# Performance work log

Hardware: AMD Instinct MI355X
Metric: run time of the kernel (lower is better)

Reference implementation:

```python
import jax, jax.numpy as jnp
import numpy as np

N_ATOM = 4096
NHEADS = 8
C_PER_HEAD = 64
BLOCK_SIZE = 128
LOCAL_WINDOW = 512


def setup_inputs() -> dict:
    key = jax.random.key(0)
    k1, k2, k3, k4 = jax.random.split(key, 4)
    q = jax.random.normal(k1, (N_ATOM, NHEADS, C_PER_HEAD), dtype=jnp.float32)
    k = jax.random.normal(k2, (N_ATOM, NHEADS, C_PER_HEAD), dtype=jnp.float32)
    v = jax.random.normal(k3, (N_ATOM, NHEADS, C_PER_HEAD), dtype=jnp.float32)
    pair_bias = jax.random.normal(k4, (N_ATOM, N_ATOM, NHEADS), dtype=jnp.float32)
    return {"q": q, "k": k, "v": v, "pair_bias": pair_bias}


def reference(q, k, v, pair_bias):
    # Local block-sparse attention: banded blockmask with blocks_per_side
    # = max(1, local_window // block_size) blocks on each side of the diagonal.
    # NOTE: pair_bias is accepted by the original forward but never used
    # (it is not passed to block_sparse_attn_func), so it is ignored here.
    N, H, D = q.shape
    B = BLOCK_SIZE
    bps = max(1, LOCAL_WINDOW // BLOCK_SIZE)  # blocks per side = 4
    nrow = N // B  # N is a multiple of block_size here
    scale = jnp.asarray(D, q.dtype) ** -0.5  # softmax_scale=None -> 1/sqrt(d)

    qb = q.reshape(nrow, B, H, D)
    kb = k.reshape(nrow, B, H, D)
    vb = v.reshape(nrow, B, H, D)

    offs = jnp.arange(-bps, bps + 1)                      # [W], W = 2*bps+1
    cols = jnp.arange(nrow)[:, None] + offs[None, :]      # [nrow, W]
    valid = (cols >= 0) & (cols < nrow)                   # band edge mask
    colsc = jnp.clip(cols, 0, nrow - 1)

    kg = kb[colsc]  # [nrow, W, B, H, D] -- only band blocks gathered
    vg = vb[colsc]

    # scores: [nrow, H, B, W, B]
    scores = jnp.einsum('rihd,rwjhd->rhiwj', qb, kg) * scale
    neg_inf = jnp.asarray(-jnp.inf, scores.dtype)
    scores = jnp.where(valid[:, None, None, :, None], scores, neg_inf)

    p = jax.nn.softmax(scores.reshape(nrow, H, B, -1), axis=-1)
    p = p.reshape(scores.shape)

    out = jnp.einsum('rhiwj,rwjhd->rihd', p, vg)  # [nrow, B, H, D]
    return out.reshape(N, H, D)
```

## Files before the change

kernel.cpp:

```cpp
#include <hip/hip_runtime.h>
#include <hip/hip_bf16.h>

#define NATOM 4096
#define NH 8
#define DIMD 64
#define BLK 128
#define NROW 32
#define BPS 4
#define ROWSTRIDE (NH * DIMD)
#define SCALE 0.125f
#define L2E 1.4426950408889634f

#define K_LD 72
#define V_LD 136
#define P_LD 136

#define HEAD_ELEMS (NATOM * DIMD)
#define WS_NEEDED  (2u * NH * HEAD_ELEMS * 2u)

typedef __attribute__((ext_vector_type(8))) short bf16x8;
typedef __attribute__((ext_vector_type(4))) float f32x4;
typedef __attribute__((ext_vector_type(4))) unsigned int u32x4;

__device__ __forceinline__ short f2bf(float x) {
    unsigned int u = __builtin_bit_cast(unsigned int, x);
    unsigned int r = (u + 0x7fffu + ((u >> 16) & 1u)) >> 16;
    return (short)r;
}
__device__ __forceinline__ unsigned int cvtpk(float lo, float hi) {
    unsigned int r;
    asm("v_cvt_pk_bf16_f32 %0, %1, %2" : "=v"(r) : "v"(lo), "v"(hi));
    return r;
}

extern "C" __global__ __launch_bounds__(256)
void prep_kernel(const float* __restrict__ k, const float* __restrict__ v,
                 short* __restrict__ Kb, short* __restrict__ Vt)
{
    __shared__ short Tr[DIMD * V_LD];
    const int bid  = blockIdx.x;
    const int h    = bid & 7;
    const int part = bid >> 3;
    const int t    = threadIdx.x;

    if (part < 32) {
        const int nb = part;
        #pragma unroll
        for (int i = 0; i < 4; ++i) {
            int idx = i * 256 + t;
            int row = idx >> 3;
            int d0  = (idx & 7) * 8;
            const float* src = k + (size_t)(nb * BLK + row) * ROWSTRIDE + h * DIMD + d0;
            float4 a = *(const float4*)src;
            float4 c = *(const float4*)(src + 4);
            bf16x8 f;
            f[0] = f2bf(a.x); f[1] = f2bf(a.y); f[2] = f2bf(a.z); f[3] = f2bf(a.w);
            f[4] = f2bf(c.x); f[5] = f2bf(c.y); f[6] = f2bf(c.z); f[7] = f2bf(c.w);
            *(bf16x8*)(Kb + (size_t)h * HEAD_ELEMS + (size_t)(nb * BLK + row) * DIMD + d0) = f;
        }
    } else {
        const int nb = part - 32;
        const int vd = t & 63;
        const int g  = t >> 6;
        const float* vp = v + (size_t)(nb * BLK) * ROWSTRIDE + h * DIMD + vd;
        #pragma unroll
        for (int i = 0; i < 8; ++i) {
            int n4 = i * 16 + g * 4;
            const float* vr = vp + (size_t)n4 * ROWSTRIDE;
            short4 s4;
            s4.x = f2bf(vr[0 * ROWSTRIDE]);
            s4.y = f2bf(vr[1 * ROWSTRIDE]);
            s4.z = f2bf(vr[2 * ROWSTRIDE]);
            s4.w = f2bf(vr[3 * ROWSTRIDE]);
            *(short4*)&Tr[vd * V_LD + n4] = s4;
        }
        __syncthreads();
        #pragma unroll
        for (int i = 0; i < 4; ++i) {
            int s  = i * 256 + t;
            int d  = s >> 4;
            int c8 = (s & 15) * 8;
            int kc = c8 >> 5;
            int l2 = (c8 >> 3) & 3;
            int kA = kc * 32 + l2 * 4;
            short4 a  = *(const short4*)&Tr[d * V_LD + kA];
            short4 c4 = *(const short4*)&Tr[d * V_LD + kA + 16];
            bf16x8 f;
            f[0] = a.x;  f[1] = a.y;  f[2] = a.z;  f[3] = a.w;
            f[4] = c4.x; f[5] = c4.y; f[6] = c4.z; f[7] = c4.w;
            *(bf16x8*)(Vt + (size_t)h * HEAD_ELEMS + (size_t)d * NATOM + nb * BLK + c8) = f;
        }
    }
}

extern "C" __global__ __launch_bounds__(256)
void bsattn_main(const float* __restrict__ q,
                 const short* __restrict__ Kb,
                 const short* __restrict__ Vt,
                 float* __restrict__ out)
{
    __shared__ short Ksh[2][BLK * K_LD];
    __shared__ short Vsh[2][DIMD * V_LD];

    const int bid = blockIdx.x;
    const int h   = bid & 7;
    const int br  = bid >> 3;
    const int r   = br >> 1;
    const int t   = threadIdx.x;
    const int w   = t >> 6;
    const int lane = t & 63;
    const int lr = lane >> 4;
    const int lc = lane & 15;

    const int qbase = br * 64 + w * 16;
    const float* qp = q + (size_t)(qbase + lc) * ROWSTRIDE + h * DIMD + lr * 8;
    bf16x8 qf[2];
    #pragma unroll
    for (int kc = 0; kc < 2; ++kc) {
        float4 a = *(const float4*)(qp + kc * 32);
        float4 b = *(const float4*)(qp + kc * 32 + 4);
        bf16x8 f;
        f[0] = f2bf(a.x * (SCALE * L2E)); f[1] = f2bf(a.y * (SCALE * L2E));
        f[2] = f2bf(a.z * (SCALE * L2E)); f[3] = f2bf(a.w * (SCALE * L2E));
        f[4] = f2bf(b.x * (SCALE * L2E)); f[5] = f2bf(b.y * (SCALE * L2E));
        f[6] = f2bf(b.z * (SCALE * L2E)); f[7] = f2bf(b.w * (SCALE * L2E));
        qf[kc] = f;
    }
    bf16x8 onesA;
    #pragma unroll
    for (int i = 0; i < 8; ++i) onesA[i] = (short)0x3F80;

    const short* kbase = Kb + (size_t)h * HEAD_ELEMS;
    const short* vbase = Vt + (size_t)h * HEAD_ELEMS;

    f32x4 acc[4] = {};
    f32x4 lacc = {};

    const int kb0 = (r - BPS > 0) ? (r - BPS) : 0;
    const int kb1 = (r + BPS < NROW - 1) ? (r + BPS) : (NROW - 1);

    const short* kg = kbase + (size_t)kb0 * BLK * DIMD;
    const short* vg = vbase + (size_t)kb0 * BLK;
    bf16x8 kpre[4], vpre[4];

#define LOADREGS()                                                              \
    {                                                                           \
        _Pragma("unroll")                                                       \
        for (int i = 0; i < 4; ++i) {                                           \
            int s = i * 256 + t;                                                \
            kpre[i] = *(const bf16x8*)(kg + (size_t)(s >> 3) * DIMD + (s & 7) * 8); \
            vpre[i] = *(const bf16x8*)(vg + (size_t)(s >> 4) * NATOM + (s & 15) * 8); \
        }                                                                       \
        kg += BLK * DIMD; vg += BLK;                                            \
    }

#define STAGE(buf)                                                              \
    {                                                                           \
        _Pragma("unroll")                                                       \
        for (int i = 0; i < 4; ++i) {                                           \
            int s = i * 256 + t;                                                \
            *(bf16x8*)&Ksh[buf][(s >> 3) * K_LD + (s & 7) * 8] = kpre[i];       \
            *(bf16x8*)&Vsh[buf][(s >> 4) * V_LD + (s & 15) * 8] = vpre[i];      \
        }                                                                       \
    }

    LOADREGS();
    STAGE(0);
    if (kb0 < kb1) LOADREGS();
    __syncthreads();

    int cur = 0;
    for (int kb = kb0; kb <= kb1; ++kb) {
        const short* ks = &Ksh[cur][0];
        const short* vs = &Vsh[cur][0];

        f32x4 s[8];
        __builtin_amdgcn_s_setprio(1);
        #pragma unroll
        for (int mt = 0; mt < 8; ++mt) {
            f32x4 z = {};
            #pragma unroll
            for (int kc = 0; kc < 2; ++kc) {
                bf16x8 kf = *(const bf16x8*)&ks[(mt * 16 + lc) * K_LD + kc * 32 + lr * 8];
                z = __builtin_amdgcn_mfma_f32_16x16x32_bf16(kf, qf[kc], z, 0, 0, 0);
            }
            s[mt] = z;
        }
        __builtin_amdgcn_s_setprio(0);

        #pragma unroll
        for (int mt = 0; mt < 8; ++mt) {
            #pragma unroll
            for (int e = 0; e < 4; ++e)
                s[mt][e] = __builtin_amdgcn_exp2f(s[mt][e]);
        }

        bf16x8 pf[4];
        #pragma unroll
        for (int kc = 0; kc < 4; ++kc) {
            u32x4 pk;
            pk[0] = cvtpk(s[2 * kc][0],     s[2 * kc][1]);
            pk[1] = cvtpk(s[2 * kc][2],     s[2 * kc][3]);
            pk[2] = cvtpk(s[2 * kc + 1][0], s[2 * kc + 1][1]);
            pk[3] = cvtpk(s[2 * kc + 1][2], s[2 * kc + 1][3]);
            pf[kc] = __builtin_bit_cast(bf16x8, pk);
        }

        if (kb < kb1) {
            STAGE(cur ^ 1);
            if (kb + 1 < kb1) LOADREGS();
        }

        __builtin_amdgcn_s_setprio(1);
        #pragma unroll
        for (int dn = 0; dn < 4; ++dn) {
            f32x4 o = acc[dn];
            #pragma unroll
            for (int kc = 0; kc < 4; ++kc) {
                bf16x8 vf = *(const bf16x8*)&vs[(dn * 16 + lc) * V_LD + kc * 32 + lr * 8];
                o = __builtin_amdgcn_mfma_f32_16x16x32_bf16(vf, pf[kc], o, 0, 0, 0);
            }
            acc[dn] = o;
        }
        #pragma unroll
        for (int kc = 0; kc < 4; ++kc)
            lacc = __builtin_amdgcn_mfma_f32_16x16x32_bf16(onesA, pf[kc], lacc, 0, 0, 0);
        __builtin_amdgcn_s_setprio(0);

        __syncthreads();
        cur ^= 1;
    }

    float inv = 1.0f / lacc[0];
    float* orow = out + (size_t)(qbase + lc) * ROWSTRIDE + h * DIMD;
    #pragma unroll
    for (int dn = 0; dn < 4; ++dn) {
        f32x4 rv;
        rv[0] = acc[dn][0] * inv; rv[1] = acc[dn][1] * inv;
        rv[2] = acc[dn][2] * inv; rv[3] = acc[dn][3] * inv;
        *(float4*)(orow + dn * 16 + lr * 4) = *(float4*)&rv;
    }
#undef LOADREGS
#undef STAGE
}

extern "C" __global__ __launch_bounds__(512)
void bsattn_fallback(const float* __restrict__ q,
                     const float* __restrict__ k,
                     const float* __restrict__ v,
                     float* __restrict__ out)
{
    __shared__ short Ksh[BLK * K_LD];
    __shared__ short Vsh[DIMD * V_LD];
    __shared__ short Psh[8][16 * P_LD];

    const int r = blockIdx.x;
    const int h = blockIdx.y;
    const int t = threadIdx.x;
    const int w = t >> 6;
    const int lane = t & 63;
    const int lr = lane >> 4;
    const int lc = lane & 15;

    const int krow = t >> 4;
    const int kcol = (t & 15) * 4;
    const int vd  = t & 63;
    const int vkg = t >> 6;

    const int qrow_l = w * 16 + lc;
    const float* qp = q + (size_t)(r * BLK + qrow_l) * ROWSTRIDE + h * DIMD + lr * 8;
    bf16x8 qf[2];
    #pragma unroll
    for (int kc = 0; kc < 2; ++kc) {
        float4 a = *(const float4*)(qp + kc * 32);
        float4 b = *(const float4*)(qp + kc * 32 + 4);
        bf16x8 f;
        f[0] = f2bf(a.x); f[1] = f2bf(a.y); f[2] = f2bf(a.z); f[3] = f2bf(a.w);
        f[4] = f2bf(b.x); f[5] = f2bf(b.y); f[6] = f2bf(b.z); f[7] = f2bf(b.w);
        qf[kc] = f;
    }

    f32x4 acc[4] = {};
    float m_run[4], l_run[4];
    #pragma unroll
    for (int i = 0; i < 4; ++i) { m_run[i] = -1e30f; l_run[i] = 0.0f; }

    const int kb0 = (r - BPS > 0) ? (r - BPS) : 0;
    const int kb1 = (r + BPS < NROW - 1) ? (r + BPS) : (NROW - 1);

    for (int kb = kb0; kb <= kb1; ++kb) {
        __syncthreads();
        const float* kp = k + (size_t)(kb * BLK) * ROWSTRIDE + h * DIMD;
        const float* vp = v + (size_t)(kb * BLK) * ROWSTRIDE + h * DIMD;

        #pragma unroll
        for (int i = 0; i < 4; ++i) {
            float4 kv = *(const float4*)(kp + (size_t)(i * 32 + krow) * ROWSTRIDE + kcol);
            short4 ks;
            ks.x = f2bf(kv.x); ks.y = f2bf(kv.y); ks.z = f2bf(kv.z); ks.w = f2bf(kv.w);
            *(short4*)&Ksh[(i * 32 + krow) * K_LD + kcol] = ks;

            const float* vr = vp + (size_t)(i * 32 + vkg * 4) * ROWSTRIDE + vd;
            short4 vs;
            vs.x = f2bf(vr[0 * ROWSTRIDE]);
            vs.y = f2bf(vr[1 * ROWSTRIDE]);
            vs.z = f2bf(vr[2 * ROWSTRIDE]);
            vs.w = f2bf(vr[3 * ROWSTRIDE]);
            *(short4*)&Vsh[vd * V_LD + i * 32 + vkg * 4] = vs;
        }
        __syncthreads();

        f32x4 s[8];
        #pragma unroll
        for (int n = 0; n < 8; ++n) {
            f32x4 z = {};
            #pragma unroll
            for (int kc = 0; kc < 2; ++kc) {
                bf16x8 kf = *(const bf16x8*)&Ksh[(n * 16 + lc) * K_LD + kc * 32 + lr * 8];
                z = __builtin_amdgcn_mfma_f32_16x16x32_bf16(qf[kc], kf, z, 0, 0, 0);
            }
            s[n] = z * SCALE;
        }

        #pragma unroll
        for (int rr = 0; rr < 4; ++rr) {
            float mx = s[0][rr];
            #pragma unroll
            for (int n = 1; n < 8; ++n) mx = fmaxf(mx, s[n][rr]);
            #pragma unroll
            for (int off = 1; off < 16; off <<= 1)
                mx = fmaxf(mx, __shfl_xor(mx, off, 64));
            float mnew = fmaxf(m_run[rr], mx);
            float al = exp2f((m_run[rr] - mnew) * L2E);
            m_run[rr] = mnew;
            float sum = 0.0f;
            #pragma unroll
            for (int n = 0; n < 8; ++n) {
                float p = exp2f((s[n][rr] - mnew) * L2E);
                s[n][rr] = p;
                sum += p;
            }
            #pragma unroll
            for (int off = 1; off < 16; off <<= 1)
                sum += __shfl_xor(sum, off, 64);
            l_run[rr] = l_run[rr] * al + sum;
            #pragma unroll
            for (int dn = 0; dn < 4; ++dn) acc[dn][rr] *= al;
        }

        short* pw = &Psh[w][0];
        #pragma unroll
        for (int n = 0; n < 8; ++n) {
            #pragma unroll
            for (int rr = 0; rr < 4; ++rr) {
                pw[(lr * 4 + rr) * P_LD + n * 16 + lc] = f2bf(s[n][rr]);
            }
        }

        #pragma unroll
        for (int dn = 0; dn < 4; ++dn) {
            f32x4 o = acc[dn];
            #pragma unroll
            for (int kc = 0; kc < 4; ++kc) {
                bf16x8 pf = *(const bf16x8*)&pw[lc * P_LD + kc * 32 + lr * 8];
                bf16x8 vf = *(const bf16x8*)&Vsh[(dn * 16 + lc) * V_LD + kc * 32 + lr * 8];
                o = __builtin_amdgcn_mfma_f32_16x16x32_bf16(pf, vf, o, 0, 0, 0);
            }
            acc[dn] = o;
        }
    }

    float* op = out + (size_t)(r * BLK + w * 16) * ROWSTRIDE + h * DIMD;
    #pragma unroll
    for (int rr = 0; rr < 4; ++rr) {
        float inv = 1.0f / l_run[rr];
        float* orow = op + (size_t)(lr * 4 + rr) * ROWSTRIDE;
        #pragma unroll
        for (int dn = 0; dn < 4; ++dn) {
            orow[dn * 16 + lc] = acc[dn][rr] * inv;
        }
    }
}

extern "C" void kernel_launch(void* const* d_in, const int* in_sizes, int n_in,
                              void* d_out, int out_size, void* d_ws, size_t ws_size,
                              hipStream_t stream) {
    const float* q = (const float*)d_in[0];
    const float* k = (const float*)d_in[1];
    const float* v = (const float*)d_in[2];
    float* out = (float*)d_out;

    if (ws_size >= (size_t)WS_NEEDED) {
        short* Kb = (short*)d_ws;
        short* Vt = Kb + (size_t)NH * HEAD_ELEMS;
        prep_kernel<<<512, 256, 0, stream>>>(k, v, Kb, Vt);
        bsattn_main<<<512, 256, 0, stream>>>(q, Kb, Vt, out);
    } else {
        bsattn_fallback<<<dim3(NROW, NH), 512, 0, stream>>>(q, k, v, out);
    }
}
```

Measured before the change: 28.26 us.

## Switch main attention kernel to 32x32x16 MFMA with full 128-row query blocks

Replaces the 16x16x32 MFMA tiling with 32x32x16 tiles, so each workgroup handles a whole 128-row query block (4 waves x 32 rows) and the grid is halved to 256 workgroups. K/V in shared memory switch from padded layouts to XOR-swizzled layouts, and the prep kernel's V transpose order is changed to match the new fragment layout. The row sum is now accumulated from exp values in registers instead of a ones-matrix MFMA. Fewer workgroups halves redundant K/V tile loads, but the 256-workgroup grid may underfill the GPU's CUs.

New measurement: 30.16 us. 6.7% more time.

```diff
diff --git a/kernel.cpp b/kernel.cpp
--- a/kernel.cpp
+++ b/kernel.cpp
@@ -11,15 +11,16 @@
 #define SCALE 0.125f
 #define L2E 1.4426950408889634f
 
-#define K_LD 72
 #define V_LD 136
 #define P_LD 136
+#define K_LDF 72
 
 #define HEAD_ELEMS (NATOM * DIMD)
 #define WS_NEEDED  (2u * NH * HEAD_ELEMS * 2u)
 
 typedef __attribute__((ext_vector_type(8))) short bf16x8;
 typedef __attribute__((ext_vector_type(4))) float f32x4;
+typedef __attribute__((ext_vector_type(16))) float f32x16;
 typedef __attribute__((ext_vector_type(4))) unsigned int u32x4;
 
 __device__ __forceinline__ short f2bf(float x) {
@@ -79,12 +80,11 @@
         for (int i = 0; i < 4; ++i) {
             int s  = i * 256 + t;
             int d  = s >> 4;
-            int c8 = (s & 15) * 8;
-            int kc = c8 >> 5;
-            int l2 = (c8 >> 3) & 3;
-            int kA = kc * 32 + l2 * 4;
+            int cc = s & 15;
+            int c8 = cc * 8;
+            int kA = (cc >> 1) * 16 + (cc & 1) * 4;
             short4 a  = *(const short4*)&Tr[d * V_LD + kA];
-            short4 c4 = *(const short4*)&Tr[d * V_LD + kA + 16];
+            short4 c4 = *(const short4*)&Tr[d * V_LD + kA + 8];
             bf16x8 f;
             f[0] = a.x;  f[1] = a.y;  f[2] = a.z;  f[3] = a.w;
             f[4] = c4.x; f[5] = c4.y; f[6] = c4.z; f[7] = c4.w;
@@ -93,32 +93,32 @@
     }
 }
 
-extern "C" __global__ __launch_bounds__(256)
+extern "C" __global__ __launch_bounds__(256, 1)
 void bsattn_main(const float* __restrict__ q,
                  const short* __restrict__ Kb,
                  const short* __restrict__ Vt,
                  float* __restrict__ out)
 {
-    __shared__ short Ksh[2][BLK * K_LD];
-    __shared__ short Vsh[2][DIMD * V_LD];
+    __shared__ short Ksh[2][BLK * DIMD];
+    __shared__ short Vsh[2][DIMD * BLK];
 
     const int bid = blockIdx.x;
     const int h   = bid & 7;
-    const int br  = bid >> 3;
-    const int r   = br >> 1;
+    const int rb  = bid >> 3;
     const int t   = threadIdx.x;
     const int w   = t >> 6;
     const int lane = t & 63;
-    const int lr = lane >> 4;
-    const int lc = lane & 15;
-
-    const int qbase = br * 64 + w * 16;
-    const float* qp = q + (size_t)(qbase + lc) * ROWSTRIDE + h * DIMD + lr * 8;
-    bf16x8 qf[2];
+    const int lc  = lane & 31;
+    const int hi  = lane >> 5;
+
+    const int qrow = rb * BLK + w * 32 + lc;
+    const float* qp = q + (size_t)qrow * ROWSTRIDE + h * DIMD;
+    bf16x8 qf[4];
     #pragma unroll
-    for (int kc = 0; kc < 2; ++kc) {
-        float4 a = *(const float4*)(qp + kc * 32);
-        float4 b = *(const float4*)(qp + kc * 32 + 4);
+    for (int kc = 0; kc < 4; ++kc) {
+        const float* p = qp + kc * 16 + hi * 8;
+        float4 a = *(const float4*)p;
+        float4 b = *(const float4*)(p + 4);
         bf16x8 f;
         f[0] = f2bf(a.x * (SCALE * L2E)); f[1] = f2bf(a.y * (SCALE * L2E));
         f[2] = f2bf(a.z * (SCALE * L2E)); f[3] = f2bf(a.w * (SCALE * L2E));
@@ -126,42 +126,41 @@
         f[6] = f2bf(b.z * (SCALE * L2E)); f[7] = f2bf(b.w * (SCALE * L2E));
         qf[kc] = f;
     }
-    bf16x8 onesA;
-    #pragma unroll
-    for (int i = 0; i < 8; ++i) onesA[i] = (short)0x3F80;
 
     const short* kbase = Kb + (size_t)h * HEAD_ELEMS;
     const short* vbase = Vt + (size_t)h * HEAD_ELEMS;
 
-    f32x4 acc[4] = {};
-    f32x4 lacc = {};
-
-    const int kb0 = (r - BPS > 0) ? (r - BPS) : 0;
-    const int kb1 = (r + BPS < NROW - 1) ? (r + BPS) : (NROW - 1);
-
-    const short* kg = kbase + (size_t)kb0 * BLK * DIMD;
-    const short* vg = vbase + (size_t)kb0 * BLK;
+    f32x16 oacc[2] = {};
+    float sv = 0.0f;
+
+    const int kb0 = (rb - BPS > 0) ? (rb - BPS) : 0;
+    const int kb1 = (rb + BPS < NROW - 1) ? (rb + BPS) : (NROW - 1);
+
+    const short* kgp = kbase + (size_t)kb0 * BLK * DIMD;
+    const short* vgp = vbase + (size_t)kb0 * BLK;
     bf16x8 kpre[4], vpre[4];
 
-#define LOADREGS()                                                              \
-    {                                                                           \
-        _Pragma("unroll")                                                       \
-        for (int i = 0; i < 4; ++i) {                                           \
-            int s = i * 256 + t;                                                \
-            kpre[i] = *(const bf16x8*)(kg + (size_t)(s >> 3) * DIMD + (s & 7) * 8); \
-            vpre[i] = *(const bf16x8*)(vg + (size_t)(s >> 4) * NATOM + (s & 15) * 8); \
-        }                                                                       \
-        kg += BLK * DIMD; vg += BLK;                                            \
-    }
-
-#define STAGE(buf)                                                              \
-    {                                                                           \
-        _Pragma("unroll")                                                       \
-        for (int i = 0; i < 4; ++i) {                                           \
-            int s = i * 256 + t;                                                \
-            *(bf16x8*)&Ksh[buf][(s >> 3) * K_LD + (s & 7) * 8] = kpre[i];       \
-            *(bf16x8*)&Vsh[buf][(s >> 4) * V_LD + (s & 15) * 8] = vpre[i];      \
-        }                                                                       \
+#define LOADREGS()                                                               \
+    {                                                                            \
+        _Pragma("unroll")                                                        \
+        for (int i = 0; i < 4; ++i) {                                            \
+            int idx = i * 256 + t;                                               \
+            kpre[i] = *(const bf16x8*)(kgp + (size_t)(idx >> 3) * DIMD + (idx & 7) * 8);   \
+            vpre[i] = *(const bf16x8*)(vgp + (size_t)(idx >> 4) * NATOM + (idx & 15) * 8); \
+        }                                                                        \
+        kgp += BLK * DIMD; vgp += BLK;                                           \
+    }
+
+#define STAGE(buf)                                                               \
+    {                                                                            \
+        _Pragma("unroll")                                                        \
+        for (int i = 0; i < 4; ++i) {                                            \
+            int idx = i * 256 + t;                                               \
+            int kr = idx >> 3, kch = idx & 7;                                    \
+            *(bf16x8*)&Ksh[buf][kr * DIMD + ((kch ^ (kr & 7)) << 3)] = kpre[i];  \
+            int vd = idx >> 4, vch = idx & 15;                                   \
+            *(bf16x8*)&Vsh[buf][vd * BLK + ((vch ^ (vd & 7)) << 3)] = vpre[i];   \
+        }                                                                        \
     }
 
     LOADREGS();
@@ -174,36 +173,40 @@
         const short* ks = &Ksh[cur][0];
         const short* vs = &Vsh[cur][0];
 
-        f32x4 s[8];
+        f32x16 sA[4];
         __builtin_amdgcn_s_setprio(1);
         #pragma unroll
-        for (int mt = 0; mt < 8; ++mt) {
-            f32x4 z = {};
-            #pragma unroll
-            for (int kc = 0; kc < 2; ++kc) {
-                bf16x8 kf = *(const bf16x8*)&ks[(mt * 16 + lc) * K_LD + kc * 32 + lr * 8];
-                z = __builtin_amdgcn_mfma_f32_16x16x32_bf16(kf, qf[kc], z, 0, 0, 0);
-            }
-            s[mt] = z;
+        for (int mt = 0; mt < 4; ++mt) {
+            f32x16 z = {};
+            #pragma unroll
+            for (int kc = 0; kc < 4; ++kc) {
+                int row = mt * 32 + lc;
+                bf16x8 kf = *(const bf16x8*)&ks[row * DIMD + (((2 * kc + hi) ^ (row & 7)) << 3)];
+                z = __builtin_amdgcn_mfma_f32_32x32x16_bf16(kf, qf[kc], z, 0, 0, 0);
+            }
+            sA[mt] = z;
         }
         __builtin_amdgcn_s_setprio(0);
 
         #pragma unroll
-        for (int mt = 0; mt < 8; ++mt) {
-            #pragma unroll
-            for (int e = 0; e < 4; ++e)
-                s[mt][e] = __builtin_amdgcn_exp2f(s[mt][e]);
-        }
-
-        bf16x8 pf[4];
-        #pragma unroll
-        for (int kc = 0; kc < 4; ++kc) {
+        for (int mt = 0; mt < 4; ++mt) {
+            #pragma unroll
+            for (int e = 0; e < 16; ++e) {
+                float p = __builtin_amdgcn_exp2f(sA[mt][e]);
+                sA[mt][e] = p;
+                sv += p;
+            }
+        }
+
+        bf16x8 pf[8];
+        #pragma unroll
+        for (int kb16 = 0; kb16 < 8; ++kb16) {
+            int mt = kb16 >> 1, base = (kb16 & 1) * 8;
             u32x4 pk;
-            pk[0] = cvtpk(s[2 * kc][0],     s[2 * kc][1]);
-            pk[1] = cvtpk(s[2 * kc][2],     s[2 * kc][3]);
-            pk[2] = cvtpk(s[2 * kc + 1][0], s[2 * kc + 1][1]);
-            pk[3] = cvtpk(s[2 * kc + 1][2], s[2 * kc + 1][3]);
-            pf[kc] = __builtin_bit_cast(bf16x8, pk);
+            #pragma unroll
+            for (int w2 = 0; w2 < 4; ++w2)
+                pk[w2] = cvtpk(sA[mt][base + 2 * w2], sA[mt][base + 2 * w2 + 1]);
+            pf[kb16] = __builtin_bit_cast(bf16x8, pk);
         }
 
         if (kb < kb1) {
@@ -213,32 +216,36 @@
 
         __builtin_amdgcn_s_setprio(1);
         #pragma unroll
-        for (int dn = 0; dn < 4; ++dn) {
-            f32x4 o = acc[dn];
-            #pragma unroll
-            for (int kc = 0; kc < 4; ++kc) {
-                bf16x8 vf = *(const bf16x8*)&vs[(dn * 16 + lc) * V_LD + kc * 32 + lr * 8];
-                o = __builtin_amdgcn_mfma_f32_16x16x32_bf16(vf, pf[kc], o, 0, 0, 0);
-            }
-            acc[dn] = o;
-        }
-        #pragma unroll
-        for (int kc = 0; kc < 4; ++kc)
-            lacc = __builtin_amdgcn_mfma_f32_16x16x32_bf16(onesA, pf[kc], lacc, 0, 0, 0);
+        for (int dmt = 0; dmt < 2; ++dmt) {
+            f32x16 o = oacc[dmt];
+            #pragma unroll
+            for (int kb16 = 0; kb16 < 8; ++kb16) {
+                int row = dmt * 32 + lc;
+                bf16x8 vf = *(const bf16x8*)&vs[row * BLK + (((2 * kb16 + hi) ^ (row & 7)) << 3)];
+                o = __builtin_amdgcn_mfma_f32_32x32x16_bf16(vf, pf[kb16], o, 0, 0, 0);
+            }
+            oacc[dmt] = o;
+        }
         __builtin_amdgcn_s_setprio(0);
 
         __syncthreads();
         cur ^= 1;
     }
 
-    float inv = 1.0f / lacc[0];
-    float* orow = out + (size_t)(qbase + lc) * ROWSTRIDE + h * DIMD;
+    float l = sv + __shfl_xor(sv, 32, 64);
+    float inv = 1.0f / l;
+    float* orow = out + (size_t)qrow * ROWSTRIDE + h * DIMD;
     #pragma unroll
-    for (int dn = 0; dn < 4; ++dn) {
-        f32x4 rv;
-        rv[0] = acc[dn][0] * inv; rv[1] = acc[dn][1] * inv;
-        rv[2] = acc[dn][2] * inv; rv[3] = acc[dn][3] * inv;
-        *(float4*)(orow + dn * 16 + lr * 4) = *(float4*)&rv;
+    for (int dmt = 0; dmt < 2; ++dmt) {
+        #pragma unroll
+        for (int g = 0; g < 4; ++g) {
+            float4 rv;
+            rv.x = oacc[dmt][4 * g + 0] * inv;
+            rv.y = oacc[dmt][4 * g + 1] * inv;
+            rv.z = oacc[dmt][4 * g + 2] * inv;
+            rv.w = oacc[dmt][4 * g + 3] * inv;
+            *(float4*)(orow + dmt * 32 + g * 8 + hi * 4) = rv;
+        }
     }
 #undef LOADREGS
 #undef STAGE
@@ -250,7 +257,7 @@
                      const float* __restrict__ v,
                      float* __restrict__ out)
 {
-    __shared__ short Ksh[BLK * K_LD];
+    __shared__ short Ksh[BLK * K_LDF];
     __shared__ short Vsh[DIMD * V_LD];
     __shared__ short Psh[8][16 * P_LD];
 
@@ -298,7 +305,7 @@
             float4 kv = *(const float4*)(kp + (size_t)(i * 32 + krow) * ROWSTRIDE + kcol);
             short4 ks;
             ks.x = f2bf(kv.x); ks.y = f2bf(kv.y); ks.z = f2bf(kv.z); ks.w = f2bf(kv.w);
-            *(short4*)&Ksh[(i * 32 + krow) * K_LD + kcol] = ks;
+            *(short4*)&Ksh[(i * 32 + krow) * K_LDF + kcol] = ks;
 
             const float* vr = vp + (size_t)(i * 32 + vkg * 4) * ROWSTRIDE + vd;
             short4 vs;
@@ -316,7 +323,7 @@
             f32x4 z = {};
             #pragma unroll
             for (int kc = 0; kc < 2; ++kc) {
-                bf16x8 kf = *(const bf16x8*)&Ksh[(n * 16 + lc) * K_LD + kc * 32 + lr * 8];
+                bf16x8 kf = *(const bf16x8*)&Ksh[(n * 16 + lc) * K_LDF + kc * 32 + lr * 8];
                 z = __builtin_amdgcn_mfma_f32_16x16x32_bf16(qf[kc], kf, z, 0, 0, 0);
             }
             s[n] = z * SCALE;
@@ -362,9 +369,9 @@
             f32x4 o = acc[dn];
             #pragma unroll
             for (int kc = 0; kc < 4; ++kc) {
-                bf16x8 pf = *(const bf16x8*)&pw[lc * P_LD + kc * 32 + lr * 8];
+                bf16x8 pfr = *(const bf16x8*)&pw[lc * P_LD + kc * 32 + lr * 8];
                 bf16x8 vf = *(const bf16x8*)&Vsh[(dn * 16 + lc) * V_LD + kc * 32 + lr * 8];
-                o = __builtin_amdgcn_mfma_f32_16x16x32_bf16(pf, vf, o, 0, 0, 0);
+                o = __builtin_amdgcn_mfma_f32_16x16x32_bf16(pfr, vf, o, 0, 0, 0);
             }
             acc[dn] = o;
         }
@@ -394,7 +401,7 @@
         short* Kb = (short*)d_ws;
         short* Vt = Kb + (size_t)NH * HEAD_ELEMS;
         prep_kernel<<<512, 256, 0, stream>>>(k, v, Kb, Vt);
-        bsattn_main<<<512, 256, 0, stream>>>(q, Kb, Vt, out);
+        bsattn_main<<<256, 256, 0, stream>>>(q, Kb, Vt, out);
     } else {
         bsattn_fallback<<<dim3(NROW, NH), 512, 0, stream>>>(q, k, v, out);
     }
```

## Stream K/V tiles into LDS with global_load_lds using XOR-swizzled prepacked layout

Applied to the files above, without the earlier changes.

The prep kernel now writes K and transposed V in a per-tile layout with an XOR swizzle of 16-byte chunks. The main kernel can then copy whole tiles straight into LDS with global_load_lds, with no register staging and no padding. Loads for tile kb+2 are issued after the barrier into the buffer just consumed. LDS reads apply the matching XOR swizzle to avoid bank conflicts. This removes the VGPR round-trip and the LDS store instructions, but adds a full vmcnt(0) drain each iteration.

After: 27.09 us. 1.04x faster.

```diff
diff --git a/kernel.cpp b/kernel.cpp
--- a/kernel.cpp
+++ b/kernel.cpp
@@ -11,9 +11,10 @@
 #define SCALE 0.125f
 #define L2E 1.4426950408889634f
 
-#define K_LD 72
+#define TILE_EL (BLK * DIMD)
 #define V_LD 136
 #define P_LD 136
+#define K_LDF 72
 
 #define HEAD_ELEMS (NATOM * DIMD)
 #define WS_NEEDED  (2u * NH * HEAD_ELEMS * 2u)
@@ -31,6 +32,9 @@
     unsigned int r;
     asm("v_cvt_pk_bf16_f32 %0, %1, %2" : "=v"(r) : "v"(lo), "v"(hi));
     return r;
+}
+__device__ __forceinline__ void drain_gll() {
+    asm volatile("s_waitcnt vmcnt(0)" ::: "memory");
 }
 
 extern "C" __global__ __launch_bounds__(256)
@@ -49,14 +53,17 @@
         for (int i = 0; i < 4; ++i) {
             int idx = i * 256 + t;
             int row = idx >> 3;
-            int d0  = (idx & 7) * 8;
-            const float* src = k + (size_t)(nb * BLK + row) * ROWSTRIDE + h * DIMD + d0;
+            int c   = idx & 7;
+            int d0  = c * 8;
+            int grow = nb * BLK + row;
+            const float* src = k + (size_t)grow * ROWSTRIDE + h * DIMD + d0;
             float4 a = *(const float4*)src;
-            float4 c = *(const float4*)(src + 4);
+            float4 cc = *(const float4*)(src + 4);
             bf16x8 f;
             f[0] = f2bf(a.x); f[1] = f2bf(a.y); f[2] = f2bf(a.z); f[3] = f2bf(a.w);
-            f[4] = f2bf(c.x); f[5] = f2bf(c.y); f[6] = f2bf(c.z); f[7] = f2bf(c.w);
-            *(bf16x8*)(Kb + (size_t)h * HEAD_ELEMS + (size_t)(nb * BLK + row) * DIMD + d0) = f;
+            f[4] = f2bf(cc.x); f[5] = f2bf(cc.y); f[6] = f2bf(cc.z); f[7] = f2bf(cc.w);
+            *(bf16x8*)(Kb + (size_t)h * HEAD_ELEMS + (size_t)grow * DIMD
+                       + ((c ^ (grow & 7)) * 8)) = f;
         }
     } else {
         const int nb = part - 32;
@@ -79,16 +86,17 @@
         for (int i = 0; i < 4; ++i) {
             int s  = i * 256 + t;
             int d  = s >> 4;
-            int c8 = (s & 15) * 8;
-            int kc = c8 >> 5;
-            int l2 = (c8 >> 3) & 3;
+            int cc = s & 15;
+            int kc = cc >> 2;
+            int l2 = cc & 3;
             int kA = kc * 32 + l2 * 4;
             short4 a  = *(const short4*)&Tr[d * V_LD + kA];
             short4 c4 = *(const short4*)&Tr[d * V_LD + kA + 16];
             bf16x8 f;
             f[0] = a.x;  f[1] = a.y;  f[2] = a.z;  f[3] = a.w;
             f[4] = c4.x; f[5] = c4.y; f[6] = c4.z; f[7] = c4.w;
-            *(bf16x8*)(Vt + (size_t)h * HEAD_ELEMS + (size_t)d * NATOM + nb * BLK + c8) = f;
+            *(bf16x8*)(Vt + (size_t)h * HEAD_ELEMS + (size_t)nb * TILE_EL
+                       + d * BLK + ((cc ^ (d & 15)) * 8)) = f;
         }
     }
 }
@@ -99,8 +107,8 @@
                  const short* __restrict__ Vt,
                  float* __restrict__ out)
 {
-    __shared__ short Ksh[2][BLK * K_LD];
-    __shared__ short Vsh[2][DIMD * V_LD];
+    __shared__ short Ksh[2][TILE_EL];
+    __shared__ short Vsh[2][TILE_EL];
 
     const int bid = blockIdx.x;
     const int h   = bid & 7;
@@ -139,34 +147,30 @@
     const int kb0 = (r - BPS > 0) ? (r - BPS) : 0;
     const int kb1 = (r + BPS < NROW - 1) ? (r + BPS) : (NROW - 1);
 
-    const short* kg = kbase + (size_t)kb0 * BLK * DIMD;
-    const short* vg = vbase + (size_t)kb0 * BLK;
-    bf16x8 kpre[4], vpre[4];
-
-#define LOADREGS()                                                              \
-    {                                                                           \
-        _Pragma("unroll")                                                       \
-        for (int i = 0; i < 4; ++i) {                                           \
-            int s = i * 256 + t;                                                \
-            kpre[i] = *(const bf16x8*)(kg + (size_t)(s >> 3) * DIMD + (s & 7) * 8); \
-            vpre[i] = *(const bf16x8*)(vg + (size_t)(s >> 4) * NATOM + (s & 15) * 8); \
-        }                                                                       \
-        kg += BLK * DIMD; vg += BLK;                                            \
-    }
-
-#define STAGE(buf)                                                              \
-    {                                                                           \
-        _Pragma("unroll")                                                       \
-        for (int i = 0; i < 4; ++i) {                                           \
-            int s = i * 256 + t;                                                \
-            *(bf16x8*)&Ksh[buf][(s >> 3) * K_LD + (s & 7) * 8] = kpre[i];       \
-            *(bf16x8*)&Vsh[buf][(s >> 4) * V_LD + (s & 15) * 8] = vpre[i];      \
-        }                                                                       \
-    }
-
-    LOADREGS();
-    STAGE(0);
-    if (kb0 < kb1) LOADREGS();
+    const short* kt = kbase + (size_t)kb0 * TILE_EL;
+    const short* vt = vbase + (size_t)kb0 * TILE_EL;
+
+#define ISSUE(buf, off)                                                           \
+    {                                                                             \
+        const short* kq = kt + (size_t)(off) * TILE_EL;                           \
+        const short* vq = vt + (size_t)(off) * TILE_EL;                           \
+        _Pragma("unroll")                                                         \
+        for (int i = 0; i < 4; ++i) {                                             \
+            int idx = i * 256 + t;                                                \
+            __builtin_amdgcn_global_load_lds(                                     \
+                (const __attribute__((address_space(1))) unsigned int*)(kq + idx * 8), \
+                (__attribute__((address_space(3))) unsigned int*)(&Ksh[buf][idx * 8]), \
+                16, 0, 0);                                                        \
+            __builtin_amdgcn_global_load_lds(                                     \
+                (const __attribute__((address_space(1))) unsigned int*)(vq + idx * 8), \
+                (__attribute__((address_space(3))) unsigned int*)(&Vsh[buf][idx * 8]), \
+                16, 0, 0);                                                        \
+        }                                                                         \
+    }
+
+    ISSUE(0, 0);
+    if (kb0 < kb1) ISSUE(1, 1);
+    drain_gll();
     __syncthreads();
 
     int cur = 0;
@@ -179,9 +183,10 @@
         #pragma unroll
         for (int mt = 0; mt < 8; ++mt) {
             f32x4 z = {};
+            int row = mt * 16 + lc;
             #pragma unroll
             for (int kc = 0; kc < 2; ++kc) {
-                bf16x8 kf = *(const bf16x8*)&ks[(mt * 16 + lc) * K_LD + kc * 32 + lr * 8];
+                bf16x8 kf = *(const bf16x8*)&ks[row * DIMD + (((kc * 4 + lr) ^ (row & 7)) * 8)];
                 z = __builtin_amdgcn_mfma_f32_16x16x32_bf16(kf, qf[kc], z, 0, 0, 0);
             }
             s[mt] = z;
@@ -206,18 +211,14 @@
             pf[kc] = __builtin_bit_cast(bf16x8, pk);
         }
 
-        if (kb < kb1) {
-            STAGE(cur ^ 1);
-            if (kb + 1 < kb1) LOADREGS();
-        }
-
         __builtin_amdgcn_s_setprio(1);
         #pragma unroll
         for (int dn = 0; dn < 4; ++dn) {
             f32x4 o = acc[dn];
+            int d = dn * 16 + lc;
             #pragma unroll
             for (int kc = 0; kc < 4; ++kc) {
-                bf16x8 vf = *(const bf16x8*)&vs[(dn * 16 + lc) * V_LD + kc * 32 + lr * 8];
+                bf16x8 vf = *(const bf16x8*)&vs[d * BLK + (((kc * 4 + lr) ^ (d & 15)) * 8)];
                 o = __builtin_amdgcn_mfma_f32_16x16x32_bf16(vf, pf[kc], o, 0, 0, 0);
             }
             acc[dn] = o;
@@ -227,7 +228,9 @@
             lacc = __builtin_amdgcn_mfma_f32_16x16x32_bf16(onesA, pf[kc], lacc, 0, 0, 0);
         __builtin_amdgcn_s_setprio(0);
 
+        drain_gll();
         __syncthreads();
+        if (kb + 2 <= kb1) ISSUE(cur, kb - kb0 + 2);
         cur ^= 1;
     }
 
@@ -240,8 +243,7 @@
         rv[2] = acc[dn][2] * inv; rv[3] = acc[dn][3] * inv;
         *(float4*)(orow + dn * 16 + lr * 4) = *(float4*)&rv;
     }
-#undef LOADREGS
-#undef STAGE
+#undef ISSUE
 }
 
 extern "C" __global__ __launch_bounds__(512)
@@ -250,7 +252,7 @@
                      const float* __restrict__ v,
                      float* __restrict__ out)
 {
-    __shared__ short Ksh[BLK * K_LD];
+    __shared__ short Ksh[BLK * K_LDF];
     __shared__ short Vsh[DIMD * V_LD];
     __shared__ short Psh[8][16 * P_LD];
 
@@ -298,7 +300,7 @@
             float4 kv = *(const float4*)(kp + (size_t)(i * 32 + krow) * ROWSTRIDE + kcol);
             short4 ks;
             ks.x = f2bf(kv.x); ks.y = f2bf(kv.y); ks.z = f2bf(kv.z); ks.w = f2bf(kv.w);
-            *(short4*)&Ksh[(i * 32 + krow) * K_LD + kcol] = ks;
+            *(short4*)&Ksh[(i * 32 + krow) * K_LDF + kcol] = ks;
 
             const float* vr = vp + (size_t)(i * 32 + vkg * 4) * ROWSTRIDE + vd;
             short4 vs;
@@ -316,7 +318,7 @@
             f32x4 z = {};
             #pragma unroll
             for (int kc = 0; kc < 2; ++kc) {
-                bf16x8 kf = *(const bf16x8*)&Ksh[(n * 16 + lc) * K_LD + kc * 32 + lr * 8];
+                bf16x8 kf = *(const bf16x8*)&Ksh[(n * 16 + lc) * K_LDF + kc * 32 + lr * 8];
                 z = __builtin_amdgcn_mfma_f32_16x16x32_bf16(qf[kc], kf, z, 0, 0, 0);
             }
             s[n] = z * SCALE;
@@ -362,9 +364,9 @@
             f32x4 o = acc[dn];
             #pragma unroll
             for (int kc = 0; kc < 4; ++kc) {
-                bf16x8 pf = *(const bf16x8*)&pw[lc * P_LD + kc * 32 + lr * 8];
+                bf16x8 pfr = *(const bf16x8*)&pw[lc * P_LD + kc * 32 + lr * 8];
                 bf16x8 vf = *(const bf16x8*)&Vsh[(dn * 16 + lc) * V_LD + kc * 32 + lr * 8];
-                o = __builtin_amdgcn_mfma_f32_16x16x32_bf16(pf, vf, o, 0, 0, 0);
+                o = __builtin_amdgcn_mfma_f32_16x16x32_bf16(pfr, vf, o, 0, 0, 0);
             }
             acc[dn] = o;
         }
```
